# Optimization experiments

Measured on AMD Instinct MI355X. Metric: run time of the kernel, lower is better.

The kernel has to match this reference:

```python
import jax, jax.numpy as jnp
import numpy as np

EPS = 1e-5

def group_norm(x, gamma, beta):
    # GroupNorm(num_groups=1) on [N, C]: normalize across channels per row
    mu = jnp.mean(x, axis=-1, keepdims=True)
    var = jnp.mean(jnp.square(x - mu), axis=-1, keepdims=True)
    return (x - mu) * jax.lax.rsqrt(var + EPS) * gamma + beta

def setup_inputs() -> dict:
    key = jax.random.key(0)
    ks = jax.random.split(key, 20)
    Nc, Nt, E, D = 100_000, 100_000, 500_000, 128
    f32 = jnp.float32
    s_in, s_rp, s_ctx = 1.0 / np.sqrt(D), 0.5, 1.0 / np.sqrt(2 * D)
    return {
        "context_feat": jax.random.normal(ks[0], (Nc, D), dtype=f32),
        "target_feat": jax.random.normal(ks[1], (Nt, D), dtype=f32),
        "context_pose": jax.random.normal(ks[2], (Nc, 4), dtype=f32),
        "target_pose": jax.random.normal(ks[3], (Nt, 4), dtype=f32),
        "hi": jax.random.randint(ks[4], (E,), 0, Nc, dtype=jnp.int32),
        "wi": jax.random.randint(ks[5], (E,), 0, Nt, dtype=jnp.int32),
        # params (stored [in, out]; equals torch Linear with transposed weight)
        "W_in": jax.random.normal(ks[6], (D, D), dtype=f32) * s_in,
        "W_rp": jax.random.normal(ks[7], (4, D), dtype=f32) * s_rp,
        "b_rp": jnp.zeros((D,), dtype=f32),
        "W_ctx1": jax.random.normal(ks[8], (2 * D, D), dtype=f32) * s_ctx,
        "g_ctx": jnp.ones((D,), dtype=f32),
        "be_ctx": jnp.zeros((D,), dtype=f32),
        "W_ctx2": jax.random.normal(ks[9], (D, D), dtype=f32) * s_in,
        "g_n": jnp.ones((D,), dtype=f32),
        "be_n": jnp.zeros((D,), dtype=f32),
        "W_m1": jax.random.normal(ks[10], (D, D), dtype=f32) * s_in,
        "g_m1": jnp.ones((D,), dtype=f32),
        "be_m1": jnp.zeros((D,), dtype=f32),
        "W_m2": jax.random.normal(ks[11], (D, D), dtype=f32) * s_in,
        "g_m2": jnp.ones((D,), dtype=f32),
        "be_m2": jnp.zeros((D,), dtype=f32),
    }

def reference(context_feat, target_feat, context_pose, target_pose, hi, wi,
              W_in, W_rp, b_rp, W_ctx1, g_ctx, be_ctx, W_ctx2,
              g_n, be_n, W_m1, g_m1, be_m1, W_m2, g_m2, be_m2):
    # relpose MLP on gathered pose deltas: [E,4] -> [E,128]
    dist_feat = jax.nn.relu((context_pose[hi] - target_pose[wi]) @ W_rp + b_rp)
    # ctx branch: concat gathered context feats with relpose -> [E,256] -> [E,128]
    ctx = jnp.concatenate([context_feat[hi], dist_feat], axis=-1)
    ctx = jax.nn.relu(group_norm(ctx @ W_ctx1, g_ctx, be_ctx)) @ W_ctx2
    # scatter-add onto projected target feats
    identity = target_feat
    tf = target_feat @ W_in
    tf = tf.at[wi].add(ctx)
    tf = jax.nn.relu(group_norm(tf, g_n, be_n))
    # output MLP (Linear+GN+ReLU, Linear+GN)
    tf = jax.nn.relu(group_norm(tf @ W_m1, g_m1, be_m1))
    tf = group_norm(tf @ W_m2, g_m2, be_m2)
    return jax.nn.relu(tf + identity)
```

## Files before the change

kernel.cpp:

```cpp
#include <hip/hip_runtime.h>

typedef __bf16 bf16_t;
typedef bf16_t bf16x4 __attribute__((ext_vector_type(4)));
typedef bf16_t bf16x8 __attribute__((ext_vector_type(8)));
typedef float floatx4 __attribute__((ext_vector_type(4)));

#define EPSF 1e-5f
#define DEV static __device__ __forceinline__

__global__ __launch_bounds__(256) void k_prep(
    const float* __restrict__ W_in, const float* __restrict__ W_ctx1,
    const float* __restrict__ W_ctx2, const float* __restrict__ W_m1,
    const float* __restrict__ W_m2, bf16_t* __restrict__ sw)
{
    int idx = blockIdx.x * 256 + threadIdx.x;
    const float* W; int base, ks;
    if (idx < 16384)      { W = W_in;   base = 0;     ks = 2; }
    else if (idx < 49152) { W = W_ctx1; base = 16384; ks = 3; }
    else if (idx < 65536) { W = W_ctx2; base = 49152; ks = 2; }
    else if (idx < 81920) { W = W_m1;   base = 65536; ks = 2; }
    else                  { W = W_m2;   base = 81920; ks = 2; }
    int local = idx - base;
    int j = local & 7, l = (local >> 3) & 63, rest = local >> 9;
    int s = rest & ((1 << ks) - 1), t = rest >> ks;
    int k = s * 32 + (l >> 4) * 8 + j;
    int n = t * 16 + (l & 15);
    sw[idx] = (bf16_t)W[k * 128 + n];
}

DEV void gn_rows(floatx4* acc, int lane, const float* __restrict__ gamma,
                 const float* __restrict__ beta, bool do_relu)
{
    int m = lane & 15;
    float s1[4] = {0.f,0.f,0.f,0.f}, s2[4] = {0.f,0.f,0.f,0.f};
#pragma unroll
    for (int t = 0; t < 8; ++t)
#pragma unroll
        for (int rr = 0; rr < 4; ++rr) { float v = acc[t][rr]; s1[rr] += v; s2[rr] += v*v; }
#pragma unroll
    for (int mask = 1; mask <= 8; mask <<= 1)
#pragma unroll
        for (int rr = 0; rr < 4; ++rr) {
            s1[rr] += __shfl_xor(s1[rr], mask);
            s2[rr] += __shfl_xor(s2[rr], mask);
        }
    float mean[4], inv[4];
#pragma unroll
    for (int rr = 0; rr < 4; ++rr) {
        mean[rr] = s1[rr] * (1.f/128.f);
        float var = s2[rr] * (1.f/128.f) - mean[rr]*mean[rr];
        inv[rr] = rsqrtf(var + EPSF);
    }
#pragma unroll
    for (int t = 0; t < 8; ++t) {
        int n = t*16 + m;
        float ga = gamma[n], be = beta[n];
#pragma unroll
        for (int rr = 0; rr < 4; ++rr) {
            float v = (acc[t][rr] - mean[rr]) * inv[rr] * ga + be;
            acc[t][rr] = do_relu ? fmaxf(v, 0.f) : v;
        }
    }
}

__global__ __launch_bounds__(256) void k_count(const int* __restrict__ wi,
                                               int* __restrict__ cnt, int E)
{
    int e = blockIdx.x * 256 + threadIdx.x;
    if (e < E) atomicAdd(&cnt[wi[e]], 1);
}

__global__ __launch_bounds__(1024) void k_scan(const int* __restrict__ cnt,
                                               int* __restrict__ off, int Nt)
{
    __shared__ int wsum[16];
    __shared__ int s_carry;
    int tid = threadIdx.x, lane = tid & 63, wid = tid >> 6;
    if (tid == 0) s_carry = 0;
    __syncthreads();
    for (int bs = 0; bs < Nt; bs += 4096) {
        int i0 = bs + tid * 4;
        int v0 = 0, v1 = 0, v2 = 0, v3 = 0;
        if (i0 + 3 < Nt) {
            int4 v = *(const int4*)(cnt + i0);
            v0 = v.x; v1 = v.y; v2 = v.z; v3 = v.w;
        } else {
            if (i0     < Nt) v0 = cnt[i0];
            if (i0 + 1 < Nt) v1 = cnt[i0+1];
            if (i0 + 2 < Nt) v2 = cnt[i0+2];
            if (i0 + 3 < Nt) v3 = cnt[i0+3];
        }
        int tot = v0 + v1 + v2 + v3;
        int x = tot;
#pragma unroll
        for (int d = 1; d < 64; d <<= 1) {
            int y = __shfl_up(x, d);
            if (lane >= d) x += y;
        }
        if (lane == 63) wsum[wid] = x;
        __syncthreads();
        if (wid == 0) {
            int wv = (lane < 16) ? wsum[lane] : 0;
#pragma unroll
            for (int d = 1; d < 16; d <<= 1) {
                int y = __shfl_up(wv, d);
                if (lane >= d) wv += y;
            }
            if (lane < 16) wsum[lane] = wv;
        }
        __syncthreads();
        int ebase = s_carry + ((wid > 0) ? wsum[wid-1] : 0) + (x - tot);
        if (i0 + 3 < Nt) {
            *(int4*)(off + i0) = make_int4(ebase, ebase+v0, ebase+v0+v1, ebase+v0+v1+v2);
        } else {
            if (i0     < Nt) off[i0]   = ebase;
            if (i0 + 1 < Nt) off[i0+1] = ebase + v0;
            if (i0 + 2 < Nt) off[i0+2] = ebase + v0 + v1;
            if (i0 + 3 < Nt) off[i0+3] = ebase + v0 + v1 + v2;
        }
        __syncthreads();
        if (tid == 0) s_carry += wsum[15];
        __syncthreads();
    }
    if (tid == 0) off[Nt] = s_carry;
}

__global__ __launch_bounds__(256) void k_edge3(
    const float* __restrict__ cfeat, const float* __restrict__ cpose,
    const float* __restrict__ tpose, const int* __restrict__ hi,
    const int* __restrict__ wi, const float* __restrict__ W_rp,
    const float* __restrict__ b_rp, const float* __restrict__ g_ctx,
    const float* __restrict__ be_ctx, const bf16_t* __restrict__ swC1,
    const int* __restrict__ off, int* __restrict__ cur,
    bf16_t* __restrict__ hbuf, int E)
{
    __shared__ alignas(16) bf16_t sH[4][2176];
    int tid = threadIdx.x, lane = tid & 63, wave = tid >> 6;
    int tb = (blockIdx.x * 4 + wave) * 16;
    int r = lane & 15, g = lane >> 4;
    int e = min(tb + r, E - 1);
    int ci = hi[e], ti = wi[e];

    bf16x8 aF[8];
    const float4* cf = (const float4*)(cfeat + (size_t)ci * 128);
#pragma unroll
    for (int s = 0; s < 4; ++s) {
        int f4 = s * 8 + g * 2;
        float4 v0 = cf[f4], v1 = cf[f4 + 1];
        aF[s] = (bf16x8){ (bf16_t)v0.x, (bf16_t)v0.y, (bf16_t)v0.z, (bf16_t)v0.w,
                          (bf16_t)v1.x, (bf16_t)v1.y, (bf16_t)v1.z, (bf16_t)v1.w };
    }
    float4 cp = ((const float4*)cpose)[ci];
    float4 tp = ((const float4*)tpose)[ti];
    float d0 = cp.x - tp.x, d1 = cp.y - tp.y, d2 = cp.z - tp.z, d3 = cp.w - tp.w;
#pragma unroll
    for (int sp = 0; sp < 4; ++sp) {
        int k0 = sp * 32 + g * 8;
        const float4* w0 = (const float4*)(W_rp + k0);
        const float4* w1 = (const float4*)(W_rp + 128 + k0);
        const float4* w2 = (const float4*)(W_rp + 256 + k0);
        const float4* w3 = (const float4*)(W_rp + 384 + k0);
        const float4* bb = (const float4*)(b_rp + k0);
        float o0,o1,o2,o3,o4,o5,o6,o7;
        {
            float4 a0=w0[0], a1=w1[0], a2=w2[0], a3=w3[0], ab=bb[0];
            o0 = fmaxf(d0*a0.x + d1*a1.x + d2*a2.x + d3*a3.x + ab.x, 0.f);
            o1 = fmaxf(d0*a0.y + d1*a1.y + d2*a2.y + d3*a3.y + ab.y, 0.f);
            o2 = fmaxf(d0*a0.z + d1*a1.z + d2*a2.z + d3*a3.z + ab.z, 0.f);
            o3 = fmaxf(d0*a0.w + d1*a1.w + d2*a2.w + d3*a3.w + ab.w, 0.f);
        }
        {
            float4 a0=w0[1], a1=w1[1], a2=w2[1], a3=w3[1], ab=bb[1];
            o4 = fmaxf(d0*a0.x + d1*a1.x + d2*a2.x + d3*a3.x + ab.x, 0.f);
            o5 = fmaxf(d0*a0.y + d1*a1.y + d2*a2.y + d3*a3.y + ab.y, 0.f);
            o6 = fmaxf(d0*a0.z + d1*a1.z + d2*a2.z + d3*a3.z + ab.z, 0.f);
            o7 = fmaxf(d0*a0.w + d1*a1.w + d2*a2.w + d3*a3.w + ab.w, 0.f);
        }
        aF[4 + sp] = (bf16x8){ (bf16_t)o0, (bf16_t)o1, (bf16_t)o2, (bf16_t)o3,
                               (bf16_t)o4, (bf16_t)o5, (bf16_t)o6, (bf16_t)o7 };
    }

    floatx4 acc[8];
#pragma unroll
    for (int t = 0; t < 8; ++t) {
        floatx4 a = {0.f,0.f,0.f,0.f};
#pragma unroll
        for (int s = 0; s < 8; ++s) {
            bf16x8 bF = *(const bf16x8*)&swC1[(size_t)((t*8 + s)*64 + lane)*8];
            a = __builtin_amdgcn_mfma_f32_16x16x32_bf16(aF[s], bF, a, 0, 0, 0);
        }
        acc[t] = a;
    }
    gn_rows(acc, lane, g_ctx, be_ctx, true);

#pragma unroll
    for (int t = 0; t < 8; ++t)
#pragma unroll
        for (int rr = 0; rr < 4; ++rr)
            sH[wave][(g*4 + rr)*136 + t*16 + r] = (bf16_t)acc[t][rr];

    int r2 = lane >> 2, c2 = lane & 3;
    bool ev2 = (tb + r2) < E;
    int ti2 = __shfl(ti, r2);
    int dst = 0;
    if (ev2 && c2 == 0) dst = off[ti2] + atomicAdd(&cur[ti2], 1);
    dst = __shfl(dst, lane & ~3);
    if (ev2) {
        bf16_t* hp = hbuf + (size_t)dst * 128 + c2 * 32;
#pragma unroll
        for (int i = 0; i < 4; ++i)
            *(bf16x8*)(hp + i*8) = *(const bf16x8*)&sH[wave][r2*136 + c2*32 + i*8];
    }
}

__global__ __launch_bounds__(256) void k_out2(
    const float* __restrict__ tfeat, const bf16_t* __restrict__ hbuf,
    const int* __restrict__ off,
    const float* __restrict__ g_n, const float* __restrict__ be_n,
    const float* __restrict__ g_m1, const float* __restrict__ be_m1,
    const float* __restrict__ g_m2, const float* __restrict__ be_m2,
    const bf16_t* __restrict__ swIn, const bf16_t* __restrict__ swC2,
    const bf16_t* __restrict__ swM1, const bf16_t* __restrict__ swM2,
    float* __restrict__ out, int Nt)
{
    __shared__ alignas(16) bf16_t sA[4][4096];
    int tid = threadIdx.x, lane = tid & 63, wave = tid >> 6;
    int tb = (blockIdx.x*4 + wave)*16;
    int r = lane >> 2, c = lane & 3, cb = c*32;
    int grow = tb + r;
    bool rv = grow < Nt;

    const float4* src = (const float4*)(tfeat + (size_t)(rv ? grow : 0)*128 + cb);
#pragma unroll
    for (int i = 0; i < 8; ++i) {
        float4 v = rv ? src[i] : make_float4(0.f,0.f,0.f,0.f);
        int k = cb + 4*i;
        int s = k >> 5, q = (k >> 3) & 3, j = k & 7;
        bf16x4 pk = { (bf16_t)v.x, (bf16_t)v.y, (bf16_t)v.z, (bf16_t)v.w };
        *(bf16x4*)&sA[wave][(s*64 + q*16 + r)*8 + j] = pk;
    }
    float sums[32];
#pragma unroll
    for (int i = 0; i < 32; ++i) sums[i] = 0.f;
    int jb = rv ? off[grow] : 0, je = rv ? off[grow+1] : 0;
    for (int jr = jb; jr < je; ++jr) {
        const bf16x8* hp = (const bf16x8*)(hbuf + (size_t)jr*128 + cb);
#pragma unroll
        for (int i = 0; i < 4; ++i) {
            bf16x8 hv = hp[i];
#pragma unroll
            for (int q = 0; q < 8; ++q) sums[i*8+q] += (float)hv[q];
        }
    }
#pragma unroll
    for (int i = 0; i < 8; ++i) {
        int k = cb + 4*i;
        int s = k >> 5, q = (k >> 3) & 3, j = k & 7;
        bf16x4 pk = { (bf16_t)sums[4*i], (bf16_t)sums[4*i+1],
                      (bf16_t)sums[4*i+2], (bf16_t)sums[4*i+3] };
        *(bf16x4*)&sA[wave][2048 + (s*64 + q*16 + r)*8 + j] = pk;
    }
    __syncthreads();
    int m = lane & 15, g = lane >> 4;
    bf16x8 aF[4], aH[4];
#pragma unroll
    for (int s = 0; s < 4; ++s) {
        aF[s] = *(const bf16x8*)&sA[wave][(s*64 + lane)*8];
        aH[s] = *(const bf16x8*)&sA[wave][2048 + (s*64 + lane)*8];
    }
    floatx4 acc[8];
#pragma unroll
    for (int t = 0; t < 8; ++t) {
        floatx4 a = {0.f,0.f,0.f,0.f};
#pragma unroll
        for (int s = 0; s < 4; ++s)
            a = __builtin_amdgcn_mfma_f32_16x16x32_bf16(aF[s],
                  *(const bf16x8*)&swIn[((t*4+s)*64 + lane)*8], a, 0, 0, 0);
#pragma unroll
        for (int s = 0; s < 4; ++s)
            a = __builtin_amdgcn_mfma_f32_16x16x32_bf16(aH[s],
                  *(const bf16x8*)&swC2[((t*4+s)*64 + lane)*8], a, 0, 0, 0);
        acc[t] = a;
    }
    gn_rows(acc, lane, g_n, be_n, true);
    __syncthreads();
#pragma unroll
    for (int t = 0; t < 8; ++t) {
        int n = t*16 + m;
        int s = n >> 5, q = (n >> 3) & 3, j = n & 7;
#pragma unroll
        for (int rr = 0; rr < 4; ++rr)
            sA[wave][(s*64 + q*16 + (g*4+rr))*8 + j] = (bf16_t)acc[t][rr];
    }
    __syncthreads();
#pragma unroll
    for (int s = 0; s < 4; ++s) aF[s] = *(const bf16x8*)&sA[wave][(s*64 + lane)*8];
#pragma unroll
    for (int t = 0; t < 8; ++t) {
        floatx4 a = {0.f,0.f,0.f,0.f};
#pragma unroll
        for (int s = 0; s < 4; ++s)
            a = __builtin_amdgcn_mfma_f32_16x16x32_bf16(aF[s],
                  *(const bf16x8*)&swM1[((t*4+s)*64 + lane)*8], a, 0, 0, 0);
        acc[t] = a;
    }
    gn_rows(acc, lane, g_m1, be_m1, true);
    __syncthreads();
#pragma unroll
    for (int t = 0; t < 8; ++t) {
        int n = t*16 + m;
        int s = n >> 5, q = (n >> 3) & 3, j = n & 7;
#pragma unroll
        for (int rr = 0; rr < 4; ++rr)
            sA[wave][(s*64 + q*16 + (g*4+rr))*8 + j] = (bf16_t)acc[t][rr];
    }
    __syncthreads();
#pragma unroll
    for (int s = 0; s < 4; ++s) aF[s] = *(const bf16x8*)&sA[wave][(s*64 + lane)*8];
#pragma unroll
    for (int t = 0; t < 8; ++t) {
        floatx4 a = {0.f,0.f,0.f,0.f};
#pragma unroll
        for (int s = 0; s < 4; ++s)
            a = __builtin_amdgcn_mfma_f32_16x16x32_bf16(aF[s],
                  *(const bf16x8*)&swM2[((t*4+s)*64 + lane)*8], a, 0, 0, 0);
        acc[t] = a;
    }
    gn_rows(acc, lane, g_m2, be_m2, false);

    __syncthreads();
    float* sF = (float*)&sA[wave][0];
#pragma unroll
    for (int t = 0; t < 8; ++t)
#pragma unroll
        for (int rr = 0; rr < 4; ++rr)
            sF[(g*4+rr)*128 + t*16 + m] = acc[t][rr];
    __syncthreads();
    const float4* idp = (const float4*)(tfeat + (size_t)tb*128);
    float4* op = (float4*)(out + (size_t)tb*128);
    const float4* sf4 = (const float4*)sF;
    int maxf = (Nt - tb < 16) ? (Nt - tb) * 32 : 512;
#pragma unroll
    for (int kk = 0; kk < 8; ++kk) {
        int f = kk*64 + lane;
        if (f < maxf) {
            float4 v = sf4[f], idv = idp[f];
            v.x = fmaxf(v.x + idv.x, 0.f);
            v.y = fmaxf(v.y + idv.y, 0.f);
            v.z = fmaxf(v.z + idv.z, 0.f);
            v.w = fmaxf(v.w + idv.w, 0.f);
            op[f] = v;
        }
    }
}

__global__ __launch_bounds__(256) void k_gemm_in(
    const float* __restrict__ tfeat, const bf16_t* __restrict__ swW,
    float* __restrict__ tf, int Nt)
{
    __shared__ alignas(16) bf16_t sA[4][2048];
    int tid = threadIdx.x, lane = tid & 63, wave = tid >> 6;

    int tb = (blockIdx.x * 4 + wave) * 16;
    int r = lane >> 2, cb = (lane & 3) * 32;
    int grow = tb + r;
    bool rv = grow < Nt;
    const float4* src = (const float4*)(tfeat + (size_t)(rv ? grow : 0) * 128 + cb);
#pragma unroll
    for (int i = 0; i < 8; ++i) {
        float4 v = rv ? src[i] : make_float4(0.f,0.f,0.f,0.f);
        int k = cb + 4*i;
        int s = k >> 5, q = (k >> 3) & 3, j = k & 7;
        bf16x4 pk = { (bf16_t)v.x, (bf16_t)v.y, (bf16_t)v.z, (bf16_t)v.w };
        *(bf16x4*)&sA[wave][(s*64 + q*16 + r)*8 + j] = pk;
    }
    __syncthreads();
    int m = lane & 15, g = lane >> 4;
    bf16x8 aF[4];
#pragma unroll
    for (int s = 0; s < 4; ++s) aF[s] = *(const bf16x8*)&sA[wave][(s*64 + lane)*8];
#pragma unroll
    for (int t = 0; t < 8; ++t) {
        floatx4 a = {0.f,0.f,0.f,0.f};
#pragma unroll
        for (int s = 0; s < 4; ++s) {
            bf16x8 bF = *(const bf16x8*)&swW[((t*4+s)*64 + lane)*8];
            a = __builtin_amdgcn_mfma_f32_16x16x32_bf16(aF[s], bF, a, 0, 0, 0);
        }
#pragma unroll
        for (int rr = 0; rr < 4; ++rr) {
            int row = tb + g*4 + rr;
            if (row < Nt) tf[(size_t)row*128 + t*16 + m] = a[rr];
        }
    }
}

__global__ __launch_bounds__(256) void k_edge_old(
    const float* __restrict__ cfeat, const float* __restrict__ cpose,
    const float* __restrict__ tpose, const int* __restrict__ hi,
    const int* __restrict__ wi, const float* __restrict__ W_rp,
    const float* __restrict__ b_rp, const float* __restrict__ g_ctx,
    const float* __restrict__ be_ctx, const bf16_t* __restrict__ swC1,
    const bf16_t* __restrict__ swC2, float* __restrict__ tf, int E)
{
    __shared__ alignas(16) bf16_t sA[4][4096];
    int tid = threadIdx.x, lane = tid & 63, wave = tid >> 6;

    int tb = (blockIdx.x * 4 + wave) * 16;
    int r = lane >> 2, cb = (lane & 3) * 32;
    int e = min(tb + r, E - 1);
    int ci = hi[e], ti = wi[e];
    const float4* src = (const float4*)(cfeat + (size_t)ci * 128 + cb);
#pragma unroll
    for (int i = 0; i < 8; ++i) {
        float4 v = src[i];
        int k = cb + 4*i;
        int s = k >> 5, q = (k >> 3) & 3, j = k & 7;
        bf16x4 pk = { (bf16_t)v.x, (bf16_t)v.y, (bf16_t)v.z, (bf16_t)v.w };
        *(bf16x4*)&sA[wave][(s*64 + q*16 + r)*8 + j] = pk;
    }
    float4 cp = ((const float4*)cpose)[ci];
    float4 tp = ((const float4*)tpose)[ti];
    float d0 = cp.x - tp.x, d1 = cp.y - tp.y, d2 = cp.z - tp.z, d3 = cp.w - tp.w;
#pragma unroll
    for (int i = 0; i < 8; ++i) {
        int cc = cb + 4*i;
        float4 w0 = *(const float4*)(W_rp + cc);
        float4 w1 = *(const float4*)(W_rp + 128 + cc);
        float4 w2 = *(const float4*)(W_rp + 256 + cc);
        float4 w3 = *(const float4*)(W_rp + 384 + cc);
        float4 bb = *(const float4*)(b_rp + cc);
        float o0 = fmaxf(d0*w0.x + d1*w1.x + d2*w2.x + d3*w3.x + bb.x, 0.f);
        float o1 = fmaxf(d0*w0.y + d1*w1.y + d2*w2.y + d3*w3.y + bb.y, 0.f);
        float o2 = fmaxf(d0*w0.z + d1*w1.z + d2*w2.z + d3*w3.z + bb.z, 0.f);
        float o3 = fmaxf(d0*w0.w + d1*w1.w + d2*w2.w + d3*w3.w + bb.w, 0.f);
        int k = 128 + cc;
        int s = k >> 5, q = (k >> 3) & 3, j = k & 7;
        bf16x4 pk = { (bf16_t)o0, (bf16_t)o1, (bf16_t)o2, (bf16_t)o3 };
        *(bf16x4*)&sA[wave][(s*64 + q*16 + r)*8 + j] = pk;
    }
    __syncthreads();

    int m = lane & 15, g = lane >> 4;
    bf16x8 aF[8];
#pragma unroll
    for (int s = 0; s < 8; ++s) aF[s] = *(const bf16x8*)&sA[wave][(s*64 + lane)*8];
    floatx4 acc[8];
#pragma unroll
    for (int t = 0; t < 8; ++t) {
        floatx4 a = {0.f,0.f,0.f,0.f};
#pragma unroll
        for (int s = 0; s < 8; ++s) {
            bf16x8 bF = *(const bf16x8*)&swC1[(size_t)((t*8+s)*64 + lane)*8];
            a = __builtin_amdgcn_mfma_f32_16x16x32_bf16(aF[s], bF, a, 0, 0, 0);
        }
        acc[t] = a;
    }
    gn_rows(acc, lane, g_ctx, be_ctx, true);
    __syncthreads();
#pragma unroll
    for (int t = 0; t < 8; ++t) {
        int n = t*16 + m;
        int s = n >> 5, q = (n >> 3) & 3, j = n & 7;
#pragma unroll
        for (int rr = 0; rr < 4; ++rr)
            sA[wave][(s*64 + q*16 + (g*4+rr))*8 + j] = (bf16_t)acc[t][rr];
    }
    __syncthreads();
    bf16x8 aF2[4];
#pragma unroll
    for (int s = 0; s < 4; ++s) aF2[s] = *(const bf16x8*)&sA[wave][(s*64 + lane)*8];
    int dstrow[4]; bool vald[4];
#pragma unroll
    for (int rr = 0; rr < 4; ++rr) {
        int ee = tb + g*4 + rr;
        vald[rr] = ee < E;
        dstrow[rr] = vald[rr] ? wi[ee] : 0;
    }
#pragma unroll
    for (int t = 0; t < 8; ++t) {
        floatx4 a = {0.f,0.f,0.f,0.f};
#pragma unroll
        for (int s = 0; s < 4; ++s) {
            bf16x8 bF = *(const bf16x8*)&swC2[((t*4+s)*64 + lane)*8];
            a = __builtin_amdgcn_mfma_f32_16x16x32_bf16(aF2[s], bF, a, 0, 0, 0);
        }
#pragma unroll
        for (int rr = 0; rr < 4; ++rr) {
            if (vald[rr])
                atomicAdd(&tf[(size_t)dstrow[rr]*128 + t*16 + m], a[rr]);
        }
    }
}

__global__ __launch_bounds__(256) void k_out_old(
    const float* __restrict__ tf, const float* __restrict__ identity,
    const float* __restrict__ g_n, const float* __restrict__ be_n,
    const float* __restrict__ g_m1, const float* __restrict__ be_m1,
    const float* __restrict__ g_m2, const float* __restrict__ be_m2,
    const bf16_t* __restrict__ swM1, const bf16_t* __restrict__ swM2,
    float* __restrict__ out, int Nt)
{
    __shared__ alignas(16) bf16_t sA[4][2048];
    int tid = threadIdx.x, lane = tid & 63, wave = tid >> 6;

    int tb = (blockIdx.x*4 + wave)*16;
    int r = lane >> 2, cb = (lane & 3)*32;
    int grow = tb + r;
    bool rv = grow < Nt;
    const float4* src = (const float4*)(tf + (size_t)(rv ? grow : 0)*128 + cb);
    float vals[32];
    float ls = 0.f, lq = 0.f;
#pragma unroll
    for (int i = 0; i < 8; ++i) {
        float4 v = rv ? src[i] : make_float4(0.f,0.f,0.f,0.f);
        vals[4*i+0]=v.x; vals[4*i+1]=v.y; vals[4*i+2]=v.z; vals[4*i+3]=v.w;
        ls += v.x+v.y+v.z+v.w;
        lq += v.x*v.x+v.y*v.y+v.z*v.z+v.w*v.w;
    }
    ls += __shfl_xor(ls,1); lq += __shfl_xor(lq,1);
    ls += __shfl_xor(ls,2); lq += __shfl_xor(lq,2);
    float mean = ls*(1.f/128.f);
    float inv = rsqrtf(lq*(1.f/128.f) - mean*mean + EPSF);
#pragma unroll
    for (int i = 0; i < 8; ++i) {
        int cc = cb + 4*i;
        float4 ga = *(const float4*)(g_n + cc);
        float4 be = *(const float4*)(be_n + cc);
        float o0 = fmaxf((vals[4*i+0]-mean)*inv*ga.x + be.x, 0.f);
        float o1 = fmaxf((vals[4*i+1]-mean)*inv*ga.y + be.y, 0.f);
        float o2 = fmaxf((vals[4*i+2]-mean)*inv*ga.z + be.z, 0.f);
        float o3 = fmaxf((vals[4*i+3]-mean)*inv*ga.w + be.w, 0.f);
        int s = cc >> 5, q = (cc >> 3) & 3, j = cc & 7;
        bf16x4 pk = { (bf16_t)o0, (bf16_t)o1, (bf16_t)o2, (bf16_t)o3 };
        *(bf16x4*)&sA[wave][(s*64 + q*16 + r)*8 + j] = pk;
    }
    __syncthreads();
    int m = lane & 15, g = lane >> 4;
    bf16x8 aF[4];
#pragma unroll
    for (int s = 0; s < 4; ++s) aF[s] = *(const bf16x8*)&sA[wave][(s*64 + lane)*8];
    floatx4 acc[8];
#pragma unroll
    for (int t = 0; t < 8; ++t) {
        floatx4 a = {0.f,0.f,0.f,0.f};
#pragma unroll
        for (int s = 0; s < 4; ++s) {
            bf16x8 bF = *(const bf16x8*)&swM1[((t*4+s)*64 + lane)*8];
            a = __builtin_amdgcn_mfma_f32_16x16x32_bf16(aF[s], bF, a, 0, 0, 0);
        }
        acc[t] = a;
    }
    gn_rows(acc, lane, g_m1, be_m1, true);
    __syncthreads();
#pragma unroll
    for (int t = 0; t < 8; ++t) {
        int n = t*16 + m;
        int s = n >> 5, q = (n >> 3) & 3, j = n & 7;
#pragma unroll
        for (int rr = 0; rr < 4; ++rr)
            sA[wave][(s*64 + q*16 + (g*4+rr))*8 + j] = (bf16_t)acc[t][rr];
    }
    __syncthreads();
#pragma unroll
    for (int s = 0; s < 4; ++s) aF[s] = *(const bf16x8*)&sA[wave][(s*64 + lane)*8];
#pragma unroll
    for (int t = 0; t < 8; ++t) {
        floatx4 a = {0.f,0.f,0.f,0.f};
#pragma unroll
        for (int s = 0; s < 4; ++s) {
            bf16x8 bF = *(const bf16x8*)&swM2[((t*4+s)*64 + lane)*8];
            a = __builtin_amdgcn_mfma_f32_16x16x32_bf16(aF[s], bF, a, 0, 0, 0);
        }
        acc[t] = a;
    }
    gn_rows(acc, lane, g_m2, be_m2, false);
#pragma unroll
    for (int t = 0; t < 8; ++t) {
        int n = t*16 + m;
#pragma unroll
        for (int rr = 0; rr < 4; ++rr) {
            int row = tb + g*4 + rr;
            if (row < Nt) {
                float v = acc[t][rr] + identity[(size_t)row*128 + n];
                out[(size_t)row*128 + n] = fmaxf(v, 0.f);
            }
        }
    }
}

extern "C" void kernel_launch(void* const* d_in, const int* in_sizes, int n_in,
                              void* d_out, int out_size, void* d_ws, size_t ws_size,
                              hipStream_t stream)
{
    const float* cfeat  = (const float*)d_in[0];
    const float* tfeat  = (const float*)d_in[1];
    const float* cpose  = (const float*)d_in[2];
    const float* tpose  = (const float*)d_in[3];
    const int*   hi     = (const int*)d_in[4];
    const int*   wi     = (const int*)d_in[5];
    const float* W_in   = (const float*)d_in[6];
    const float* W_rp   = (const float*)d_in[7];
    const float* b_rp   = (const float*)d_in[8];
    const float* W_ctx1 = (const float*)d_in[9];
    const float* g_ctx  = (const float*)d_in[10];
    const float* be_ctx = (const float*)d_in[11];
    const float* W_ctx2 = (const float*)d_in[12];
    const float* g_n    = (const float*)d_in[13];
    const float* be_n   = (const float*)d_in[14];
    const float* W_m1   = (const float*)d_in[15];
    const float* g_m1   = (const float*)d_in[16];
    const float* be_m1  = (const float*)d_in[17];
    const float* W_m2   = (const float*)d_in[18];
    const float* g_m2   = (const float*)d_in[19];
    const float* be_m2  = (const float*)d_in[20];

    int Nt = in_sizes[1] / 128;
    int E  = in_sizes[4];
    float* outp = (float*)d_out;

    char* base = (char*)d_ws;
    size_t o = 98304 * sizeof(bf16_t);
    o = (o + 255) & ~(size_t)255;
    size_t o_cnt = o; o += (size_t)Nt * 4;
    o = (o + 255) & ~(size_t)255;
    size_t o_off = o; o += ((size_t)Nt + 1) * 4;
    o = (o + 255) & ~(size_t)255;
    size_t o_cur = o; o += (size_t)Nt * 4;
    o = (o + 255) & ~(size_t)255;
    size_t o_h = o; o += (size_t)E * 128 * sizeof(bf16_t);

    if (ws_size >= o) {
        bf16_t* sw   = (bf16_t*)base;
        int*    cnt  = (int*)(base + o_cnt);
        int*    off  = (int*)(base + o_off);
        int*    cur  = (int*)(base + o_cur);
        bf16_t* hbuf = (bf16_t*)(base + o_h);
        bf16_t* swIn = sw;
        bf16_t* swC1 = sw + 16384;
        bf16_t* swC2 = sw + 49152;
        bf16_t* swM1 = sw + 65536;
        bf16_t* swM2 = sw + 81920;

        hipMemsetAsync(cnt, 0, (size_t)Nt * 4, stream);
        hipMemsetAsync(cur, 0, (size_t)Nt * 4, stream);
        k_prep<<<384, 256, 0, stream>>>(W_in, W_ctx1, W_ctx2, W_m1, W_m2, sw);
        k_count<<<(E + 255) / 256, 256, 0, stream>>>(wi, cnt, E);
        k_scan<<<1, 1024, 0, stream>>>(cnt, off, Nt);
        k_edge3<<<(E + 63) / 64, 256, 0, stream>>>(cfeat, cpose, tpose, hi, wi,
                                                   W_rp, b_rp, g_ctx, be_ctx,
                                                   swC1, off, cur, hbuf, E);
        k_out2<<<(Nt + 63) / 64, 256, 0, stream>>>(tfeat, hbuf, off,
                                                   g_n, be_n, g_m1, be_m1,
                                                   g_m2, be_m2,
                                                   swIn, swC2, swM1, swM2,
                                                   outp, Nt);
    } else {
        float*  tf = (float*)d_ws;
        bf16_t* sw = (bf16_t*)((char*)d_ws + (size_t)Nt * 128 * sizeof(float));
        bf16_t* swIn = sw;
        bf16_t* swC1 = sw + 16384;
        bf16_t* swC2 = sw + 49152;
        bf16_t* swM1 = sw + 65536;
        bf16_t* swM2 = sw + 81920;

        k_prep<<<384, 256, 0, stream>>>(W_in, W_ctx1, W_ctx2, W_m1, W_m2, sw);
        k_gemm_in<<<(Nt + 63) / 64, 256, 0, stream>>>(tfeat, swIn, tf, Nt);
        k_edge_old<<<(E + 63) / 64, 256, 0, stream>>>(cfeat, cpose, tpose, hi, wi,
                                                      W_rp, b_rp, g_ctx, be_ctx,
                                                      swC1, swC2, tf, E);
        k_out_old<<<(Nt + 63) / 64, 256, 0, stream>>>(tf, tfeat, g_n, be_n,
                                                      g_m1, be_m1, g_m2, be_m2,
                                                      swM1, swM2, outp, Nt);
    }
}
```

Measured before the change: 506.3 us.

## Restructure edge and output kernels for lower register pressure and higher occupancy

The edge kernel now builds each A-fragment on the fly and accumulates all eight output tiles per K-slice, so it no longer holds eight A-fragments at once. The context-feature loads are software-prefetched one slice ahead, and `wi` is reloaded rather than shuffled. The output kernel drops the block-wide syncthreads, uses a smaller padded per-wave LDS buffer, and builds tfeat fragments directly from global memory. It also writes the final residual ReLU straight from accumulators with scalar stores instead of staging through LDS. Launch bounds of 8 blocks are added to push occupancy, at the risk of register spills and less coalesced scalar output stores.

```diff
diff --git a/kernel.cpp b/kernel.cpp
--- a/kernel.cpp
+++ b/kernel.cpp
@@ -125,7 +125,7 @@
     if (tid == 0) off[Nt] = s_carry;
 }
 
-__global__ __launch_bounds__(256) void k_edge3(
+__global__ __launch_bounds__(256, 8) void k_edge4(
     const float* __restrict__ cfeat, const float* __restrict__ cpose,
     const float* __restrict__ tpose, const int* __restrict__ hi,
     const int* __restrict__ wi, const float* __restrict__ W_rp,
@@ -141,15 +141,13 @@
     int e = min(tb + r, E - 1);
     int ci = hi[e], ti = wi[e];
 
-    bf16x8 aF[8];
+    floatx4 acc[8];
+#pragma unroll
+    for (int t = 0; t < 8; ++t) acc[t] = (floatx4){0.f,0.f,0.f,0.f};
+
     const float4* cf = (const float4*)(cfeat + (size_t)ci * 128);
-#pragma unroll
-    for (int s = 0; s < 4; ++s) {
-        int f4 = s * 8 + g * 2;
-        float4 v0 = cf[f4], v1 = cf[f4 + 1];
-        aF[s] = (bf16x8){ (bf16_t)v0.x, (bf16_t)v0.y, (bf16_t)v0.z, (bf16_t)v0.w,
-                          (bf16_t)v1.x, (bf16_t)v1.y, (bf16_t)v1.z, (bf16_t)v1.w };
-    }
+    float4 p0 = cf[g*2], p1 = cf[g*2 + 1];
+
     float4 cp = ((const float4*)cpose)[ci];
     float4 tp = ((const float4*)tpose)[ti];
     float d0 = cp.x - tp.x, d1 = cp.y - tp.y, d2 = cp.z - tp.z, d3 = cp.w - tp.w;
@@ -176,20 +174,26 @@
             o6 = fmaxf(d0*a0.z + d1*a1.z + d2*a2.z + d3*a3.z + ab.z, 0.f);
             o7 = fmaxf(d0*a0.w + d1*a1.w + d2*a2.w + d3*a3.w + ab.w, 0.f);
         }
-        aF[4 + sp] = (bf16x8){ (bf16_t)o0, (bf16_t)o1, (bf16_t)o2, (bf16_t)o3,
-                               (bf16_t)o4, (bf16_t)o5, (bf16_t)o6, (bf16_t)o7 };
-    }
-
-    floatx4 acc[8];
-#pragma unroll
-    for (int t = 0; t < 8; ++t) {
-        floatx4 a = {0.f,0.f,0.f,0.f};
-#pragma unroll
-        for (int s = 0; s < 8; ++s) {
+        bf16x8 aF = { (bf16_t)o0, (bf16_t)o1, (bf16_t)o2, (bf16_t)o3,
+                      (bf16_t)o4, (bf16_t)o5, (bf16_t)o6, (bf16_t)o7 };
+        int s = 4 + sp;
+#pragma unroll
+        for (int t = 0; t < 8; ++t) {
             bf16x8 bF = *(const bf16x8*)&swC1[(size_t)((t*8 + s)*64 + lane)*8];
-            a = __builtin_amdgcn_mfma_f32_16x16x32_bf16(aF[s], bF, a, 0, 0, 0);
-        }
-        acc[t] = a;
+            acc[t] = __builtin_amdgcn_mfma_f32_16x16x32_bf16(aF, bF, acc[t], 0, 0, 0);
+        }
+    }
+#pragma unroll
+    for (int s = 0; s < 4; ++s) {
+        float4 v0 = p0, v1 = p1;
+        if (s < 3) { p0 = cf[(s+1)*8 + g*2]; p1 = cf[(s+1)*8 + g*2 + 1]; }
+        bf16x8 aF = { (bf16_t)v0.x, (bf16_t)v0.y, (bf16_t)v0.z, (bf16_t)v0.w,
+                      (bf16_t)v1.x, (bf16_t)v1.y, (bf16_t)v1.z, (bf16_t)v1.w };
+#pragma unroll
+        for (int t = 0; t < 8; ++t) {
+            bf16x8 bF = *(const bf16x8*)&swC1[(size_t)((t*8 + s)*64 + lane)*8];
+            acc[t] = __builtin_amdgcn_mfma_f32_16x16x32_bf16(aF, bF, acc[t], 0, 0, 0);
+        }
     }
     gn_rows(acc, lane, g_ctx, be_ctx, true);
 
@@ -200,10 +204,13 @@
             sH[wave][(g*4 + rr)*136 + t*16 + r] = (bf16_t)acc[t][rr];
 
     int r2 = lane >> 2, c2 = lane & 3;
-    bool ev2 = (tb + r2) < E;
-    int ti2 = __shfl(ti, r2);
+    int e2 = tb + r2;
+    bool ev2 = e2 < E;
     int dst = 0;
-    if (ev2 && c2 == 0) dst = off[ti2] + atomicAdd(&cur[ti2], 1);
+    if (ev2 && c2 == 0) {
+        int t2 = wi[e2];
+        dst = off[t2] + atomicAdd(&cur[t2], 1);
+    }
     dst = __shfl(dst, lane & ~3);
     if (ev2) {
         bf16_t* hp = hbuf + (size_t)dst * 128 + c2 * 32;
@@ -213,7 +220,7 @@
     }
 }
 
-__global__ __launch_bounds__(256) void k_out2(
+__global__ __launch_bounds__(256, 8) void k_out3(
     const float* __restrict__ tfeat, const bf16_t* __restrict__ hbuf,
     const int* __restrict__ off,
     const float* __restrict__ g_n, const float* __restrict__ be_n,
@@ -223,133 +230,107 @@
     const bf16_t* __restrict__ swM1, const bf16_t* __restrict__ swM2,
     float* __restrict__ out, int Nt)
 {
-    __shared__ alignas(16) bf16_t sA[4][4096];
+    __shared__ alignas(16) bf16_t sB[4][2176];
     int tid = threadIdx.x, lane = tid & 63, wave = tid >> 6;
     int tb = (blockIdx.x*4 + wave)*16;
-    int r = lane >> 2, c = lane & 3, cb = c*32;
+    int r = lane & 15, g = lane >> 4;
     int grow = tb + r;
     bool rv = grow < Nt;
-
-    const float4* src = (const float4*)(tfeat + (size_t)(rv ? grow : 0)*128 + cb);
-#pragma unroll
-    for (int i = 0; i < 8; ++i) {
-        float4 v = rv ? src[i] : make_float4(0.f,0.f,0.f,0.f);
-        int k = cb + 4*i;
-        int s = k >> 5, q = (k >> 3) & 3, j = k & 7;
-        bf16x4 pk = { (bf16_t)v.x, (bf16_t)v.y, (bf16_t)v.z, (bf16_t)v.w };
-        *(bf16x4*)&sA[wave][(s*64 + q*16 + r)*8 + j] = pk;
-    }
+    int rclamp = rv ? grow : (Nt - 1);
+
     float sums[32];
 #pragma unroll
     for (int i = 0; i < 32; ++i) sums[i] = 0.f;
     int jb = rv ? off[grow] : 0, je = rv ? off[grow+1] : 0;
     for (int jr = jb; jr < je; ++jr) {
-        const bf16x8* hp = (const bf16x8*)(hbuf + (size_t)jr*128 + cb);
-#pragma unroll
-        for (int i = 0; i < 4; ++i) {
-            bf16x8 hv = hp[i];
-#pragma unroll
-            for (int q = 0; q < 8; ++q) sums[i*8+q] += (float)hv[q];
-        }
-    }
-#pragma unroll
-    for (int i = 0; i < 8; ++i) {
-        int k = cb + 4*i;
-        int s = k >> 5, q = (k >> 3) & 3, j = k & 7;
-        bf16x4 pk = { (bf16_t)sums[4*i], (bf16_t)sums[4*i+1],
-                      (bf16_t)sums[4*i+2], (bf16_t)sums[4*i+3] };
-        *(bf16x4*)&sA[wave][2048 + (s*64 + q*16 + r)*8 + j] = pk;
-    }
-    __syncthreads();
-    int m = lane & 15, g = lane >> 4;
-    bf16x8 aF[4], aH[4];
+        const bf16_t* hp = hbuf + (size_t)jr*128 + g*8;
+#pragma unroll
+        for (int s = 0; s < 4; ++s) {
+            bf16x8 hv = *(const bf16x8*)(hp + s*32);
+#pragma unroll
+            for (int q = 0; q < 8; ++q) sums[s*8+q] += (float)hv[q];
+        }
+    }
 #pragma unroll
     for (int s = 0; s < 4; ++s) {
-        aF[s] = *(const bf16x8*)&sA[wave][(s*64 + lane)*8];
-        aH[s] = *(const bf16x8*)&sA[wave][2048 + (s*64 + lane)*8];
-    }
+        bf16x8 ah = { (bf16_t)sums[s*8+0], (bf16_t)sums[s*8+1],
+                      (bf16_t)sums[s*8+2], (bf16_t)sums[s*8+3],
+                      (bf16_t)sums[s*8+4], (bf16_t)sums[s*8+5],
+                      (bf16_t)sums[s*8+6], (bf16_t)sums[s*8+7] };
+        *(bf16x8*)&sB[wave][r*136 + s*32 + g*8] = ah;
+    }
+
     floatx4 acc[8];
 #pragma unroll
-    for (int t = 0; t < 8; ++t) {
-        floatx4 a = {0.f,0.f,0.f,0.f};
-#pragma unroll
-        for (int s = 0; s < 4; ++s)
-            a = __builtin_amdgcn_mfma_f32_16x16x32_bf16(aF[s],
-                  *(const bf16x8*)&swIn[((t*4+s)*64 + lane)*8], a, 0, 0, 0);
-#pragma unroll
-        for (int s = 0; s < 4; ++s)
-            a = __builtin_amdgcn_mfma_f32_16x16x32_bf16(aH[s],
-                  *(const bf16x8*)&swC2[((t*4+s)*64 + lane)*8], a, 0, 0, 0);
-        acc[t] = a;
+    for (int t = 0; t < 8; ++t) acc[t] = (floatx4){0.f,0.f,0.f,0.f};
+    const float4* cf = (const float4*)(tfeat + (size_t)rclamp * 128);
+    float4 p0 = cf[g*2], p1 = cf[g*2 + 1];
+#pragma unroll
+    for (int s = 0; s < 4; ++s) {
+        bf16x8 aH = *(const bf16x8*)&sB[wave][r*136 + s*32 + g*8];
+#pragma unroll
+        for (int t = 0; t < 8; ++t) {
+            bf16x8 bF = *(const bf16x8*)&swC2[((t*4+s)*64 + lane)*8];
+            acc[t] = __builtin_amdgcn_mfma_f32_16x16x32_bf16(aH, bF, acc[t], 0, 0, 0);
+        }
+        float4 v0 = p0, v1 = p1;
+        if (s < 3) { p0 = cf[(s+1)*8 + g*2]; p1 = cf[(s+1)*8 + g*2 + 1]; }
+        bf16x8 aF = { (bf16_t)v0.x, (bf16_t)v0.y, (bf16_t)v0.z, (bf16_t)v0.w,
+                      (bf16_t)v1.x, (bf16_t)v1.y, (bf16_t)v1.z, (bf16_t)v1.w };
+#pragma unroll
+        for (int t = 0; t < 8; ++t) {
+            bf16x8 bF = *(const bf16x8*)&swIn[((t*4+s)*64 + lane)*8];
+            acc[t] = __builtin_amdgcn_mfma_f32_16x16x32_bf16(aF, bF, acc[t], 0, 0, 0);
+        }
     }
     gn_rows(acc, lane, g_n, be_n, true);
-    __syncthreads();
-#pragma unroll
-    for (int t = 0; t < 8; ++t) {
-        int n = t*16 + m;
-        int s = n >> 5, q = (n >> 3) & 3, j = n & 7;
+
+#pragma unroll
+    for (int t = 0; t < 8; ++t)
 #pragma unroll
         for (int rr = 0; rr < 4; ++rr)
-            sA[wave][(s*64 + q*16 + (g*4+rr))*8 + j] = (bf16_t)acc[t][rr];
-    }
-    __syncthreads();
-#pragma unroll
-    for (int s = 0; s < 4; ++s) aF[s] = *(const bf16x8*)&sA[wave][(s*64 + lane)*8];
-#pragma unroll
-    for (int t = 0; t < 8; ++t) {
-        floatx4 a = {0.f,0.f,0.f,0.f};
-#pragma unroll
-        for (int s = 0; s < 4; ++s)
-            a = __builtin_amdgcn_mfma_f32_16x16x32_bf16(aF[s],
-                  *(const bf16x8*)&swM1[((t*4+s)*64 + lane)*8], a, 0, 0, 0);
-        acc[t] = a;
+            sB[wave][(g*4 + rr)*136 + t*16 + r] = (bf16_t)acc[t][rr];
+#pragma unroll
+    for (int t = 0; t < 8; ++t) acc[t] = (floatx4){0.f,0.f,0.f,0.f};
+#pragma unroll
+    for (int s = 0; s < 4; ++s) {
+        bf16x8 aF = *(const bf16x8*)&sB[wave][r*136 + s*32 + g*8];
+#pragma unroll
+        for (int t = 0; t < 8; ++t) {
+            bf16x8 bF = *(const bf16x8*)&swM1[((t*4+s)*64 + lane)*8];
+            acc[t] = __builtin_amdgcn_mfma_f32_16x16x32_bf16(aF, bF, acc[t], 0, 0, 0);
+        }
     }
     gn_rows(acc, lane, g_m1, be_m1, true);
-    __syncthreads();
-#pragma unroll
-    for (int t = 0; t < 8; ++t) {
-        int n = t*16 + m;
-        int s = n >> 5, q = (n >> 3) & 3, j = n & 7;
+
+#pragma unroll
+    for (int t = 0; t < 8; ++t)
 #pragma unroll
         for (int rr = 0; rr < 4; ++rr)
-            sA[wave][(s*64 + q*16 + (g*4+rr))*8 + j] = (bf16_t)acc[t][rr];
-    }
-    __syncthreads();
-#pragma unroll
-    for (int s = 0; s < 4; ++s) aF[s] = *(const bf16x8*)&sA[wave][(s*64 + lane)*8];
-#pragma unroll
-    for (int t = 0; t < 8; ++t) {
-        floatx4 a = {0.f,0.f,0.f,0.f};
-#pragma unroll
-        for (int s = 0; s < 4; ++s)
-            a = __builtin_amdgcn_mfma_f32_16x16x32_bf16(aF[s],
-                  *(const bf16x8*)&swM2[((t*4+s)*64 + lane)*8], a, 0, 0, 0);
-        acc[t] = a;
+            sB[wave][(g*4 + rr)*136 + t*16 + r] = (bf16_t)acc[t][rr];
+#pragma unroll
+    for (int t = 0; t < 8; ++t) acc[t] = (floatx4){0.f,0.f,0.f,0.f};
+#pragma unroll
+    for (int s = 0; s < 4; ++s) {
+        bf16x8 aF = *(const bf16x8*)&sB[wave][r*136 + s*32 + g*8];
+#pragma unroll
+        for (int t = 0; t < 8; ++t) {
+            bf16x8 bF = *(const bf16x8*)&swM2[((t*4+s)*64 + lane)*8];
+            acc[t] = __builtin_amdgcn_mfma_f32_16x16x32_bf16(aF, bF, acc[t], 0, 0, 0);
+        }
     }
     gn_rows(acc, lane, g_m2, be_m2, false);
 
-    __syncthreads();
-    float* sF = (float*)&sA[wave][0];
-#pragma unroll
-    for (int t = 0; t < 8; ++t)
-#pragma unroll
-        for (int rr = 0; rr < 4; ++rr)
-            sF[(g*4+rr)*128 + t*16 + m] = acc[t][rr];
-    __syncthreads();
-    const float4* idp = (const float4*)(tfeat + (size_t)tb*128);
-    float4* op = (float4*)(out + (size_t)tb*128);
-    const float4* sf4 = (const float4*)sF;
-    int maxf = (Nt - tb < 16) ? (Nt - tb) * 32 : 512;
-#pragma unroll
-    for (int kk = 0; kk < 8; ++kk) {
-        int f = kk*64 + lane;
-        if (f < maxf) {
-            float4 v = sf4[f], idv = idp[f];
-            v.x = fmaxf(v.x + idv.x, 0.f);
-            v.y = fmaxf(v.y + idv.y, 0.f);
-            v.z = fmaxf(v.z + idv.z, 0.f);
-            v.w = fmaxf(v.w + idv.w, 0.f);
-            op[f] = v;
+#pragma unroll
+    for (int t = 0; t < 8; ++t) {
+        int n = t*16 + r;
+#pragma unroll
+        for (int rr = 0; rr < 4; ++rr) {
+            int row = tb + g*4 + rr;
+            if (row < Nt) {
+                float v = acc[t][rr] + tfeat[(size_t)row*128 + n];
+                out[(size_t)row*128 + n] = fmaxf(v, 0.f);
+            }
         }
     }
 }
@@ -647,10 +628,10 @@
         k_prep<<<384, 256, 0, stream>>>(W_in, W_ctx1, W_ctx2, W_m1, W_m2, sw);
         k_count<<<(E + 255) / 256, 256, 0, stream>>>(wi, cnt, E);
         k_scan<<<1, 1024, 0, stream>>>(cnt, off, Nt);
-        k_edge3<<<(E + 63) / 64, 256, 0, stream>>>(cfeat, cpose, tpose, hi, wi,
+        k_edge4<<<(E + 63) / 64, 256, 0, stream>>>(cfeat, cpose, tpose, hi, wi,
                                                    W_rp, b_rp, g_ctx, be_ctx,
                                                    swC1, off, cur, hbuf, E);
-        k_out2<<<(Nt + 63) / 64, 256, 0, stream>>>(tfeat, hbuf, off,
+        k_out3<<<(Nt + 63) / 64, 256, 0, stream>>>(tfeat, hbuf, off,
                                                    g_n, be_n, g_m1, be_m1,
                                                    g_m2, be_m2,
                                                    swIn, swC2, swM1, swM2,
```

Measured after the change: 814.5 us. 1.61x slower.
